# Performance work log

Hardware: AMD Instinct MI355X
Metric: run time of the kernel (lower is better)

## Reference

```python
import jax, jax.numpy as jnp
import numpy as np

M, D, NI, L, NPL, R, T = 2, 128, 131072, 4, 2048, 8, 32
N = NI + L * NPL  # total DAG nodes


def setup_inputs() -> dict:
    key = jax.random.key(0)
    ks = jax.random.split(key, 18)
    thax = jax.random.randint(ks[0], (NI,), 0, T)
    sine = jax.random.uniform(ks[1], (NI,), jnp.float32)
    # parents of layer-l deriv nodes index any node built earlier (topological)
    raw = jax.random.randint(ks[2], (L, NPL, 2), 0, 2**30)
    bounds = jnp.array([NI + l * NPL for l in range(L)])[:, None, None]
    par = raw % bounds
    ridx = jax.random.randint(ks[3], (L, NPL), 0, R)
    pos = jax.random.uniform(ks[4], (N,), jnp.float32) + 0.01
    neg = jax.random.uniform(ks[5], (N,), jnp.float32) + 0.01
    s = 0.05
    return {
        'thax': thax, 'sine': sine, 'par': par, 'ridx': ridx,
        'pos': pos, 'neg': neg,
        'init_table': jax.random.normal(ks[6], (M, T, D)) * s,
        's_vec': jax.random.normal(ks[7], (M, D)) * s,
        'W1': jax.random.normal(ks[8], (M, R, 2 * D, D)) * s,
        'b1': jax.random.normal(ks[9], (M, R, D)) * s,
        'W2': jax.random.normal(ks[10], (M, R, D, D)) * s,
        'b2': jax.random.normal(ks[11], (M, R, D)) * s,
        'tweaks': jax.random.normal(ks[12], (M, 1, 2)) * s,
        'We1': jax.random.normal(ks[13], (M, D, D)) * s,
        'be1': jax.random.normal(ks[14], (M, D)) * s,
        'we2': jax.random.normal(ks[15], (M, D)) * s,
        'be2': jax.random.normal(ks[16], (M,)) * s,
    }


def reference(thax, sine, par, ridx, pos, neg, init_table, s_vec,
              W1, b1, W2, b2, tweaks, We1, be1, we2, be2):
    # init nodes: thax embedding + sine embellishment (per model)
    emb0 = init_table[:, thax, :] + sine[None, :, None] * s_vec[:, None, :]  # [M,NI,D]
    store = jnp.zeros((M, N, D), emb0.dtype).at[:, :NI].set(emb0)
    # topological layers of deriv nodes: gather parents, rule-indexed 2-layer MLP
    for l in range(L):
        p, r = par[l], ridx[l]
        cat = store[:, p].reshape(M, NPL, 2 * D)               # gather parents
        h = jax.nn.relu(jnp.einsum('mnc,mncd->mnd', cat, W1[:, r]) + b1[:, r])
        out = (jnp.einsum('mnd,mnde->mne', h, W2[:, r]) + b2[:, r]
               + tweaks[:, 0, 1][:, None, None])
        store = store.at[:, NI + l * NPL: NI + (l + 1) * NPL].set(out)
    # eval_net: per-node scalar logit (+ per-problem tweak)
    he = jax.nn.relu(jnp.einsum('mnd,mde->mne', store, We1) + be1[:, None, :])
    logit = jnp.einsum('mnd,md->mn', he, we2) + be2[:, None] + tweaks[:, 0, 0][:, None]
    tot_pos, tot_neg = pos.sum(), neg.sum()
    pw = tot_neg / tot_pos  # POS_WEIGHT_EXTRA = 1.0
    gold = pos / (pos + neg)
    w = pos + neg
    # BCEWithLogitsLoss(pos_weight=pw) per node, weighted by (pos+neg)
    bce = -(pw * gold[None] * jax.nn.log_sigmoid(logit)
            + (1.0 - gold[None]) * jax.nn.log_sigmoid(-logit))
    loss = (w[None] * bce).sum(axis=1)                          # [M]
    posOK = jnp.where(logit >= 0, pos[None], 0.0).sum(axis=1)
    negOK = jnp.where(logit < 0, neg[None], 0.0).sum(axis=1)
    return (loss, posOK, negOK, tot_pos, tot_neg)
```

## Files before the change

### kernel.cpp

```cpp
#include <hip/hip_runtime.h>
#include <hip/hip_bf16.h>

#define M_ 2
#define D_ 128
#define NI_ 131072
#define L_ 4
#define NPL_ 2048
#define R_ 8
#define T_ 32
#define N_ (NI_ + L_ * NPL_)
#define ND_ (L_ * NPL_)
#define PSTRIDE_ 1792
#define PUSED_ 1665
#define FCAP_ 1280
#define SCAP_ 512
#define CCAP_ 24

typedef __bf16 bf16x8 __attribute__((ext_vector_type(8)));
typedef float f32x4 __attribute__((ext_vector_type(4)));
typedef unsigned short u16x4 __attribute__((ext_vector_type(4)));

#define OFF_W2T    0u
#define OFF_WE1T   524288u
#define OFF_TAB    589824u
#define OFF_SVEC   606208u
#define OFF_EA2    606720u
#define OFF_EWB    639488u
#define OFF_PA     641536u
#define OFF_PB     655872u
#define OFF_PPOK   670208u
#define OFF_PNOK   684544u
#define OFF_PTP    698880u
#define OFF_PTN    706048u
#define OFF_G      713216u
#define OFF_FLIST  1253888u
#define OFF_SLIST  1294848u
#define OFF_CFG    1296896u

__device__ __forceinline__ unsigned short f2bu(float f) {
  unsigned int u = __float_as_uint(f);
  u += 0x7fffu + ((u >> 16) & 1u);
  return (unsigned short)(u >> 16);
}
__device__ __forceinline__ float bfu2f(unsigned short u) {
  return __uint_as_float((unsigned int)u << 16);
}
__device__ __forceinline__ bf16x8 ldb8(const unsigned short* p) {
  return *reinterpret_cast<const bf16x8*>(p);
}

__global__ __launch_bounds__(256) void megaprep_kernel(
    const float* W1, const float* W2, const float* We1,
    const float* init_table, const float* s_vec,
    const float* b1, const float* be1, const float* we2,
    const int* ridx, const int* par,
    unsigned short* W2T, unsigned short* We1T,
    unsigned short* tab, unsigned short* svec,
    float* G, float* EA2, float* EWB,
    int* fastlist, int* slowlist, int* cfg, unsigned int* pzero) {
  __shared__ float smem[1056];
  __shared__ int lcnt;
  int job = blockIdx.x;
  int tid = threadIdx.x;

  if (job < 9) {
    int* out; int cap;
    if (job < 8) { out = fastlist + job * FCAP_; cap = FCAP_; }
    else         { out = slowlist;               cap = SCAP_; }
    if (tid == 0) lcnt = 0;
    __syncthreads();
    int lane = tid & 63;
    unsigned long long lmask_lt = (1ull << lane) - 1ull;
    for (int g = tid; g < ND_; g += 256) {
      int p0 = par[2 * g], p1 = par[2 * g + 1];
      bool fast = (p0 < NI_) && (p1 < NI_);
      bool match = (job < 8) ? (fast && ridx[g] == job) : (!fast);
      unsigned long long mask = __ballot(match);
      if (mask) {
        int leader = __ffsll((unsigned long long)mask) - 1;
        int pre = __popcll(mask & lmask_lt);
        int base_ = 0;
        if (lane == leader) base_ = atomicAdd(&lcnt, __popcll(mask));
        base_ = __shfl(base_, leader, 64);
        if (match) {
          int idx = base_ + pre;
          if (idx < cap) out[idx] = g;
        }
      }
    }
    __syncthreads();
    if (tid == 0) {
      int c = lcnt; if (c > cap) c = cap;
      cfg[job] = c;
    }
  } else if (job == 9) {
    for (int i = tid; i < 17920; i += 256) pzero[i] = 0u;
  } else if (job == 10) {
    for (int i = tid; i < 8448; i += 256) {
      if (i < 8192) tab[i] = f2bu(init_table[i]);
      else svec[i - 8192] = f2bu(s_vec[i - 8192]);
    }
  } else if (job < 45) {
    int q = job - 11;
    int m = q / 17, t = (q % 17) * 2 + (tid >> 7);
    int e = tid & 127;
    if (t <= 32) {
      const float* vec = (t < 32) ? &init_table[(size_t)(m * T_ + t) * D_]
                                  : &s_vec[(size_t)m * D_];
      const float* w = &We1[(size_t)m * D_ * D_];
      float acc = 0.f;
#pragma unroll 8
      for (int d = 0; d < 128; ++d) acc = fmaf(vec[d], w[d * D_ + e], acc);
      if (t < 32) {
        EA2[m * 4096 + ((e >> 1) * 32 + t) * 2 + (e & 1)] = acc + be1[m * D_ + e];
      } else {
        EWB[(m * D_ + e) * 2 + 0] = acc;
        EWB[(m * D_ + e) * 2 + 1] = we2[m * D_ + e];
      }
    }
  } else if (job < 573) {
    int q = job - 45;
    int t = q / 16, mr = q & 15;
    int m = mr >> 3;
    int slot = tid >> 7, e = tid & 127;
    const float* vec = (t < 32) ? &init_table[(size_t)(m * T_ + t) * D_]
                                : &s_vec[(size_t)m * D_];
    if (tid < 128) smem[tid] = vec[tid];
    __syncthreads();
    const float* w = &W1[((size_t)mr * 256 + slot * 128) * D_];
    float acc = 0.f;
#pragma unroll 8
    for (int c = 0; c < 128; ++c) acc = fmaf(smem[c], w[c * D_ + e], acc);
    if (slot == 0 && t < 32) acc += b1[mr * D_ + e];
    G[((size_t)(mr * 2 + slot) * 33 + t) * D_ + e] = acc;
  } else {
    int q0 = job - 573;
    const float* src; unsigned short* dst;
    int rblk, cblk;
    if (q0 < 256) {
      int z = q0 >> 4;
      src = W2 + (size_t)z * 16384; dst = W2T + (size_t)z * 16384;
      rblk = (q0 & 15) >> 2; cblk = q0 & 3;
    } else {
      int q = q0 - 256; int z = q >> 4;
      src = We1 + (size_t)z * 16384; dst = We1T + (size_t)z * 16384;
      rblk = (q & 15) >> 2; cblk = q & 3;
    }
    int r0 = rblk * 32, c0 = cblk * 32;
    float (*tile)[33] = (float(*)[33])smem;
    int tx = tid & 31, ty = tid >> 5;
#pragma unroll
    for (int k = 0; k < 4; ++k)
      tile[ty + 8 * k][tx] = src[(size_t)(r0 + ty + 8 * k) * D_ + c0 + tx];
    __syncthreads();
#pragma unroll
    for (int k = 0; k < 4; ++k)
      dst[(size_t)(c0 + ty + 8 * k) * D_ + r0 + tx] = f2bu(tile[tx][ty + 8 * k]);
  }
}

__global__ __launch_bounds__(256) void main_kernel(
    const int* thax, const float* sine, const int* par, const int* ridx,
    const float* pos, const float* neg,
    const float* W1, const float* b1, const float* b2, const float* tweaks,
    const float* G, const unsigned short* W2T, const unsigned short* We1T,
    const unsigned short* tab, const unsigned short* svec,
    const float* EA2, const float* EWB,
    const float* be1, const float* we2, const float* be2,
    const int* cfg, const int* fastlist, const int* slowlist,
    float* pA, float* pB, float* pPok, float* pNok, float* pTp, float* pTn) {
  __shared__ float sbuf[4448];
  int bid = blockIdx.x;
  int tid = threadIdx.x;
  int w = tid >> 6, lane = tid & 63;

  if (bid < 1280) {
    int m = bid / 640, q = bid % 640;
    int r = q / 80, tile = q % 80;
    int cnt = cfg[r];
    int base = tile * 16;
    if (base >= cnt) return;
    unsigned short* h_lds = (unsigned short*)sbuf;
    int*   t0a  = (int*)(sbuf + 1024);
    int*   t1a  = t0a + 16;
    float* s0a  = (float*)(t1a + 16);
    float* s1a  = s0a + 16;
    int*   gida = (int*)(s1a + 16);
    float* red2 = sbuf + 1104;
    if (tid < 16) {
      int loc = base + tid; if (loc >= cnt) loc = cnt - 1;
      int gid = fastlist[r * FCAP_ + loc];
      int p0 = par[2 * gid], p1 = par[2 * gid + 1];
      t0a[tid] = thax[p0]; s0a[tid] = sine[p0];
      t1a[tid] = thax[p1]; s1a[tid] = sine[p1];
      gida[tid] = gid;
    }
    __syncthreads();
    const float* Gm = &G[(size_t)(m * R_ + r) * 8448];
    {
      int row = tid >> 4, seg = tid & 15, d0 = seg * 8;
      int t0 = t0a[row], t1 = t1a[row];
      float s0 = s0a[row], s1 = s1a[row];
      const float* pa = &Gm[t0 * 128 + d0];
      const float* pb = &Gm[(33 + t1) * 128 + d0];
      const float* pu = &Gm[4096 + d0];
      const float* pv = &Gm[8320 + d0];
      bf16x8 hv;
#pragma unroll
      for (int half = 0; half < 2; ++half) {
        float4 a = *(const float4*)(pa + half * 4);
        float4 b = *(const float4*)(pb + half * 4);
        float4 u = *(const float4*)(pu + half * 4);
        float4 v = *(const float4*)(pv + half * 4);
        hv[half * 4 + 0] = (__bf16)fmaxf(a.x + b.x + s0 * u.x + s1 * v.x, 0.f);
        hv[half * 4 + 1] = (__bf16)fmaxf(a.y + b.y + s0 * u.y + s1 * v.y, 0.f);
        hv[half * 4 + 2] = (__bf16)fmaxf(a.z + b.z + s0 * u.z + s1 * v.z, 0.f);
        hv[half * 4 + 3] = (__bf16)fmaxf(a.w + b.w + s0 * u.w + s1 * v.w, 0.f);
      }
      *(bf16x8*)&h_lds[row * 128 + (d0 ^ ((row & 7) << 3))] = hv;
    }
    __syncthreads();
    int l15 = lane & 15, l4 = lane >> 4;
    const unsigned short* w2b = &W2T[(size_t)(m * R_ + r) * D_ * D_];
    f32x4 acc[2];
    acc[0] = (f32x4){0.f, 0.f, 0.f, 0.f};
    acc[1] = (f32x4){0.f, 0.f, 0.f, 0.f};
#pragma unroll
    for (int kc = 0; kc < 4; ++kc) {
      int d0 = kc * 32 + l4 * 8;
      bf16x8 a2 = ldb8(&h_lds[l15 * 128 + (d0 ^ ((l15 & 7) << 3))]);
#pragma unroll
      for (int f = 0; f < 2; ++f) {
        int fg = w * 2 + f;
        bf16x8 b = ldb8(&w2b[(fg * 16 + l15) * D_ + d0]);
        acc[f] = __builtin_amdgcn_mfma_f32_16x16x32_bf16(a2, b, acc[f], 0, 0, 0);
      }
    }
    float tw1 = tweaks[m * 2 + 1];
    const float* b2v = &b2[(m * R_ + r) * D_];
    __syncthreads();
#pragma unroll
    for (int i = 0; i < 4; ++i) {
      int row = l4 * 4 + i;
#pragma unroll
      for (int f = 0; f < 2; ++f) {
        int e = (w * 2 + f) * 16 + l15;
        h_lds[row * 128 + (e ^ ((row & 7) << 3))] = f2bu(acc[f][i] + b2v[e] + tw1);
      }
    }
    __syncthreads();
    f32x4 ae[2];
    ae[0] = (f32x4){0.f, 0.f, 0.f, 0.f};
    ae[1] = (f32x4){0.f, 0.f, 0.f, 0.f};
    const unsigned short* we1b = &We1T[(size_t)m * D_ * D_];
#pragma unroll
    for (int kc = 0; kc < 4; ++kc) {
      int d0 = kc * 32 + l4 * 8;
      bf16x8 a2 = ldb8(&h_lds[l15 * 128 + (d0 ^ ((l15 & 7) << 3))]);
#pragma unroll
      for (int f = 0; f < 2; ++f) {
        int fg = w * 2 + f;
        bf16x8 b = ldb8(&we1b[(fg * 16 + l15) * D_ + d0]);
        ae[f] = __builtin_amdgcn_mfma_f32_16x16x32_bf16(a2, b, ae[f], 0, 0, 0);
      }
    }
    float part[4] = {0.f, 0.f, 0.f, 0.f};
#pragma unroll
    for (int f = 0; f < 2; ++f) {
      int e = (w * 2 + f) * 16 + l15;
      float bb = be1[m * D_ + e];
      float wv = we2[m * D_ + e];
#pragma unroll
      for (int i = 0; i < 4; ++i) {
        float he = ae[f][i] + bb;
        he = he > 0.f ? he : 0.f;
        part[i] += he * wv;
      }
    }
#pragma unroll
    for (int mask = 1; mask < 16; mask <<= 1) {
#pragma unroll
      for (int i = 0; i < 4; ++i) part[i] += __shfl_xor(part[i], mask, 64);
    }
    if (l15 == 0) {
#pragma unroll
      for (int i = 0; i < 4; ++i) red2[w * 16 + l4 * 4 + i] = part[i];
    }
    __syncthreads();
    if (tid < 16) {
      int g = base + tid;
      float v6[4] = {0.f, 0.f, 0.f, 0.f};
      if (g < cnt) {
        float logit = red2[tid] + red2[16 + tid] + red2[32 + tid] + red2[48 + tid]
                    + be2[m] + tweaks[m * 2 + 0];
        int grow = NI_ + gida[tid];
        float p_ = pos[grow], n_ = neg[grow];
        float lse = log1pf(__expf(-fabsf(logit)));
        v6[0] = p_ * (fmaxf(-logit, 0.f) + lse);
        v6[1] = n_ * (fmaxf(logit, 0.f) + lse);
        v6[2] = logit >= 0.f ? p_ : 0.f;
        v6[3] = logit < 0.f ? n_ : 0.f;
      }
#pragma unroll
      for (int mask = 1; mask < 16; mask <<= 1) {
#pragma unroll
        for (int qq = 0; qq < 4; ++qq) v6[qq] += __shfl_xor(v6[qq], mask, 64);
      }
      if (tid == 0) {
        int slot = 512 + r * 80 + tile;
        pA[m * PSTRIDE_ + slot] = v6[0];
        pB[m * PSTRIDE_ + slot] = v6[1];
        pPok[m * PSTRIDE_ + slot] = v6[2];
        pNok[m * PSTRIDE_ + slot] = v6[3];
      }
    }
  } else if (bid < 2304) {
    int q = bid - 1280;
    int m = q >> 9, xb = q & 511;
    float* lea = sbuf;
    float* lwb = sbuf + 4096;
    float* red = sbuf + 4352;
    for (int i = tid; i < 4096; i += 256) lea[i] = EA2[m * 4096 + i];
    if (tid < 256) lwb[tid] = EWB[m * 256 + tid];
    __syncthreads();
    int row = xb * 256 + tid;
    int t = thax[row];
    float s = sine[row];
    float acc = 0.f;
#pragma unroll 8
    for (int p = 0; p < 64; ++p) {
      float2 ea = *(const float2*)&lea[(p * 32 + t) * 2];
      float4 wb = *(const float4*)&lwb[p * 4];
      float x0 = fmaf(s, wb.x, ea.x); x0 = fmaxf(x0, 0.f);
      acc = fmaf(x0, wb.y, acc);
      float x1 = fmaf(s, wb.z, ea.y); x1 = fmaxf(x1, 0.f);
      acc = fmaf(x1, wb.w, acc);
    }
    float logit = acc + be2[m] + tweaks[m * 2 + 0];
    float p_ = pos[row], n_ = neg[row];
    float lse = log1pf(__expf(-fabsf(logit)));
    float v[6];
    v[0] = p_ * (fmaxf(-logit, 0.f) + lse);
    v[1] = n_ * (fmaxf(logit, 0.f) + lse);
    v[2] = logit >= 0.f ? p_ : 0.f;
    v[3] = logit < 0.f ? n_ : 0.f;
    v[4] = p_; v[5] = n_;
#pragma unroll
    for (int mask = 1; mask < 64; mask <<= 1) {
#pragma unroll
      for (int k = 0; k < 6; ++k) v[k] += __shfl_xor(v[k], mask, 64);
    }
    if (lane == 0) {
#pragma unroll
      for (int k = 0; k < 6; ++k) red[k * 16 + w] = v[k];
    }
    __syncthreads();
    if (tid == 0) {
      float t6[6];
#pragma unroll
      for (int k = 0; k < 6; ++k)
        t6[k] = red[k * 16 + 0] + red[k * 16 + 1] + red[k * 16 + 2] + red[k * 16 + 3];
      pA[m * PSTRIDE_ + xb] = t6[0];
      pB[m * PSTRIDE_ + xb] = t6[1];
      pPok[m * PSTRIDE_ + xb] = t6[2];
      pNok[m * PSTRIDE_ + xb] = t6[3];
      if (m == 0) { pTp[xb] = t6[4]; pTn[xb] = t6[5]; }
    }
  } else if (bid < 2306) {
    int j = bid - 2304;
    float* red = sbuf;
    const float* src = j ? neg : pos;
    float s = 0.f;
    for (int i = NI_ + tid; i < N_; i += 256) s += src[i];
#pragma unroll
    for (int mask = 1; mask < 64; mask <<= 1) s += __shfl_xor(s, mask, 64);
    if (lane == 0) red[w] = s;
    __syncthreads();
    if (tid == 0) {
      float t = red[0] + red[1] + red[2] + red[3];
      if (j == 0) pTp[1152] = t; else pTn[1152] = t;
    }
  } else {
    int q = bid - 2306;
    int m = q >> 9, si = q & 511;
    if (si >= cfg[8]) return;
    int*   list  = (int*)sbuf;
    int*   meta  = (int*)(sbuf + 24);
    unsigned short* catl = (unsigned short*)(sbuf + 32);
    float* hbuf  = sbuf + 160;
    float* hp0   = sbuf + 288;
    float* hp1   = sbuf + 416;
    unsigned short* cache = (unsigned short*)(sbuf + 544);

    int g_row = slowlist[si];
    if (tid == 0) {
      int nn = 0;
      list[nn++] = g_row;
      for (int i = 0; i < nn; ++i) {
        int g = list[i];
        for (int s = 0; s < 2; ++s) {
          int p = par[2 * g + s];
          if (p >= NI_) {
            int pg = p - NI_;
            bool found = false;
            for (int jj = 0; jj < nn; ++jj) if (list[jj] == pg) { found = true; break; }
            if (!found && nn < CCAP_) list[nn++] = pg;
          }
        }
      }
      for (int i = 1; i < nn; ++i) {
        int v = list[i]; int jj = i - 1;
        while (jj >= 0 && list[jj] > v) { list[jj + 1] = list[jj]; --jj; }
        list[jj + 1] = v;
      }
      meta[0] = nn;
    }
    __syncthreads();
    int NN = meta[0];
    float tw1 = tweaks[m * 2 + 1];
    for (int j = 0; j < NN; ++j) {
      int g = list[j];
      int r = ridx[g];
      int p0 = par[2 * g], p1 = par[2 * g + 1];
      bool fastn = (p0 < NI_) && (p1 < NI_);
      if (fastn) {
        if (tid < 128) {
          int d = tid;
          const float* Gm = &G[(size_t)(m * R_ + r) * 8448];
          float hv = Gm[thax[p0] * 128 + d] + Gm[(33 + thax[p1]) * 128 + d]
                   + sine[p0] * Gm[4096 + d] + sine[p1] * Gm[8320 + d];
          hbuf[d] = bfu2f(f2bu(fmaxf(hv, 0.f)));
        }
        __syncthreads();
      } else {
        if (tid == 0) {
          int s0 = -1, s1 = -1;
          if (p0 >= NI_) for (int jj = 0; jj < j; ++jj) if (list[jj] == p0 - NI_) { s0 = jj; break; }
          if (p1 >= NI_) for (int jj = 0; jj < j; ++jj) if (list[jj] == p1 - NI_) { s1 = jj; break; }
          meta[1] = s0; meta[2] = s1;
        }
        __syncthreads();
        {
          int c = tid; int p = (c < 128) ? p0 : p1; int cc = c & 127;
          int slot = (c < 128) ? meta[1] : meta[2];
          unsigned short v;
          if (p < NI_) {
            float tv = bfu2f(tab[(m * T_ + thax[p]) * D_ + cc])
                     + sine[p] * bfu2f(svec[m * D_ + cc]);
            v = f2bu(tv);
          } else {
            v = cache[slot * 128 + cc];
          }
          catl[c] = v;
        }
        __syncthreads();
        int d = tid & 127, half = tid >> 7;
        const float* w1r = &W1[(((size_t)(m * R_ + r)) * 256 + half * 128) * D_];
        float acc = 0.f;
#pragma unroll 8
        for (int c = 0; c < 128; ++c)
          acc = fmaf(bfu2f(catl[half * 128 + c]), w1r[(size_t)c * D_ + d], acc);
        if (half == 0) hp0[d] = acc; else hp1[d] = acc;
        __syncthreads();
        if (tid < 128) {
          float hv = b1[(m * R_ + r) * D_ + tid] + hp0[tid] + hp1[tid];
          hbuf[tid] = bfu2f(f2bu(fmaxf(hv, 0.f)));
        }
        __syncthreads();
      }
      {
        int e = tid & 127, half = tid >> 7;
        const u16x4* w2r4 = (const u16x4*)&W2T[((size_t)(m * R_ + r) * D_ + e) * D_ + half * 64];
        float acc = 0.f;
#pragma unroll
        for (int dd = 0; dd < 16; ++dd) {
          u16x4 wv = w2r4[dd];
          int db = half * 64 + dd * 4;
          acc = fmaf(bfu2f(wv[0]), hbuf[db + 0], acc);
          acc = fmaf(bfu2f(wv[1]), hbuf[db + 1], acc);
          acc = fmaf(bfu2f(wv[2]), hbuf[db + 2], acc);
          acc = fmaf(bfu2f(wv[3]), hbuf[db + 3], acc);
        }
        if (half == 0) hp0[e] = acc; else hp1[e] = acc;
      }
      __syncthreads();
      if (tid < 128) {
        float o = hp0[tid] + hp1[tid] + b2[(m * R_ + r) * D_ + tid] + tw1;
        cache[j * 128 + tid] = f2bu(o);
      }
      __syncthreads();
    }
    int jr = NN - 1;
    {
      int e = tid & 127, half = tid >> 7;
      const u16x4* wer4 = (const u16x4*)&We1T[((size_t)m * D_ + e) * D_ + half * 64];
      float acc = 0.f;
#pragma unroll
      for (int dd = 0; dd < 16; ++dd) {
        u16x4 wv = wer4[dd];
        int db = half * 64 + dd * 4;
        acc = fmaf(bfu2f(wv[0]), bfu2f(cache[jr * 128 + db + 0]), acc);
        acc = fmaf(bfu2f(wv[1]), bfu2f(cache[jr * 128 + db + 1]), acc);
        acc = fmaf(bfu2f(wv[2]), bfu2f(cache[jr * 128 + db + 2]), acc);
        acc = fmaf(bfu2f(wv[3]), bfu2f(cache[jr * 128 + db + 3]), acc);
      }
      if (half == 0) hp0[e] = acc; else hp1[e] = acc;
    }
    __syncthreads();
    if (tid < 128) {
      float he = hp0[tid] + hp1[tid] + be1[m * D_ + tid];
      he = he > 0.f ? he : 0.f;
      hbuf[tid] = he * we2[m * D_ + tid];
    }
    __syncthreads();
    if (tid < 64) {
      float s = hbuf[tid] + hbuf[tid + 64];
#pragma unroll
      for (int mask = 1; mask < 64; mask <<= 1) s += __shfl_xor(s, mask, 64);
      if (tid == 0) {
        float logit = s + be2[m] + tweaks[m * 2 + 0];
        int grow = NI_ + g_row;
        float p_ = pos[grow], n_ = neg[grow];
        float lse = log1pf(__expf(-fabsf(logit)));
        int slot = 1153 + si;
        pA[m * PSTRIDE_ + slot] = p_ * (fmaxf(-logit, 0.f) + lse);
        pB[m * PSTRIDE_ + slot] = n_ * (fmaxf(logit, 0.f) + lse);
        pPok[m * PSTRIDE_ + slot] = logit >= 0.f ? p_ : 0.f;
        pNok[m * PSTRIDE_ + slot] = logit < 0.f ? n_ : 0.f;
      }
    }
  }
}

__global__ __launch_bounds__(256) void finalize_kernel(
    const float* pA, const float* pB, const float* pPok, const float* pNok,
    const float* pTp, const float* pTn, float* out) {
  __shared__ float lred[10][4];
  const float* srcs[10] = {pA, pA + PSTRIDE_, pB, pB + PSTRIDE_,
                           pPok, pPok + PSTRIDE_, pNok, pNok + PSTRIDE_,
                           pTp, pTn};
  int tid = threadIdx.x;
  int w = tid >> 6, lane = tid & 63;
#pragma unroll
  for (int q = 0; q < 10; ++q) {
    float s = 0.f;
    for (int i = tid; i < PUSED_; i += 256) s += srcs[q][i];
#pragma unroll
    for (int mask = 1; mask < 64; mask <<= 1) s += __shfl_xor(s, mask, 64);
    if (lane == 0) lred[q][w] = s;
  }
  __syncthreads();
  if (tid == 0) {
    float totals[10];
#pragma unroll
    for (int q = 0; q < 10; ++q)
      totals[q] = lred[q][0] + lred[q][1] + lred[q][2] + lred[q][3];
    float tp = totals[8], tn = totals[9];
    float pw = tn / tp;
    out[0] = pw * totals[0] + totals[2];
    out[1] = pw * totals[1] + totals[3];
    out[2] = totals[4]; out[3] = totals[5];
    out[4] = totals[6]; out[5] = totals[7];
    out[6] = tp; out[7] = tn;
  }
}

extern "C" void kernel_launch(void* const* d_in, const int* in_sizes, int n_in,
                              void* d_out, int out_size, void* d_ws, size_t ws_size,
                              hipStream_t stream) {
  const int*   thax = (const int*)d_in[0];
  const float* sine = (const float*)d_in[1];
  const int*   par  = (const int*)d_in[2];
  const int*   ridx = (const int*)d_in[3];
  const float* pos  = (const float*)d_in[4];
  const float* neg  = (const float*)d_in[5];
  const float* init_table = (const float*)d_in[6];
  const float* s_vec = (const float*)d_in[7];
  const float* W1 = (const float*)d_in[8];
  const float* b1 = (const float*)d_in[9];
  const float* W2 = (const float*)d_in[10];
  const float* b2 = (const float*)d_in[11];
  const float* tweaks = (const float*)d_in[12];
  const float* We1 = (const float*)d_in[13];
  const float* be1 = (const float*)d_in[14];
  const float* we2 = (const float*)d_in[15];
  const float* be2 = (const float*)d_in[16];

  char* ws = (char*)d_ws;
  unsigned short* W2T  = (unsigned short*)(ws + OFF_W2T);
  unsigned short* We1T = (unsigned short*)(ws + OFF_WE1T);
  unsigned short* tab  = (unsigned short*)(ws + OFF_TAB);
  unsigned short* svec = (unsigned short*)(ws + OFF_SVEC);
  float* EA2  = (float*)(ws + OFF_EA2);
  float* EWB  = (float*)(ws + OFF_EWB);
  float* pA   = (float*)(ws + OFF_PA);
  float* pB   = (float*)(ws + OFF_PB);
  float* pPok = (float*)(ws + OFF_PPOK);
  float* pNok = (float*)(ws + OFF_PNOK);
  float* pTp  = (float*)(ws + OFF_PTP);
  float* pTn  = (float*)(ws + OFF_PTN);
  float* G    = (float*)(ws + OFF_G);
  int* fastlist = (int*)(ws + OFF_FLIST);
  int* slowlist = (int*)(ws + OFF_SLIST);
  int* cfg      = (int*)(ws + OFF_CFG);

  megaprep_kernel<<<861, 256, 0, stream>>>(
      W1, W2, We1, init_table, s_vec, b1, be1, we2, ridx, par,
      W2T, We1T, tab, svec, G, EA2, EWB,
      fastlist, slowlist, cfg, (unsigned int*)pA);
  main_kernel<<<3330, 256, 0, stream>>>(
      thax, sine, par, ridx, pos, neg, W1, b1, b2, tweaks,
      G, W2T, We1T, tab, svec, EA2, EWB, be1, we2, be2,
      cfg, fastlist, slowlist,
      pA, pB, pPok, pNok, pTp, pTn);
  finalize_kernel<<<1, 256, 0, stream>>>(pA, pB, pPok, pNok, pTp, pTn,
                                         (float*)d_out);
}
```

Before: 92.43 us.

## Process slow-path dependency chains one per wavefront instead of one per block

The slow path, which recomputes each deep-layer node's ancestor chain, now gives each 64-lane wavefront its own chain and LDS slice. Block-wide __syncthreads are replaced by per-wave lgkmcnt waits, and the grid for that section shrinks fourfold. This is meant to cut barrier overhead and idle threads on the latency-bound serial chains. In exchange each lane does longer serial dot products (256- and 128-length loops), and the chain cap drops from 24 to 16, which could truncate deep chains.

Result: slower. 112.1 us (+21.3%).

```diff
diff --git a/kernel.cpp b/kernel.cpp
--- a/kernel.cpp
+++ b/kernel.cpp
@@ -14,11 +14,11 @@
 #define PUSED_ 1665
 #define FCAP_ 1280
 #define SCAP_ 512
-#define CCAP_ 24
+#define CCAP_ 16
+#define WSL_ 1312
 
 typedef __bf16 bf16x8 __attribute__((ext_vector_type(8)));
 typedef float f32x4 __attribute__((ext_vector_type(4)));
-typedef unsigned short u16x4 __attribute__((ext_vector_type(4)));
 
 #define OFF_W2T    0u
 #define OFF_WE1T   524288u
@@ -48,6 +48,10 @@
 __device__ __forceinline__ bf16x8 ldb8(const unsigned short* p) {
   return *reinterpret_cast<const bf16x8*>(p);
 }
+#define WAVE_FENCE() do { \
+  asm volatile("s_waitcnt lgkmcnt(0)" ::: "memory"); \
+  __builtin_amdgcn_sched_barrier(0); \
+} while (0)
 
 __global__ __launch_bounds__(256) void megaprep_kernel(
     const float* W1, const float* W2, const float* We1,
@@ -169,7 +173,7 @@
     const float* be1, const float* we2, const float* be2,
     const int* cfg, const int* fastlist, const int* slowlist,
     float* pA, float* pB, float* pPok, float* pNok, float* pTp, float* pTn) {
-  __shared__ float sbuf[4448];
+  __shared__ float sbuf[4 * WSL_];
   int bid = blockIdx.x;
   int tid = threadIdx.x;
   int w = tid >> 6, lane = tid & 63;
@@ -381,153 +385,122 @@
       if (j == 0) pTp[1152] = t; else pTn[1152] = t;
     }
   } else {
-    int q = bid - 2306;
-    int m = q >> 9, si = q & 511;
+    int widx = (bid - 2306) * 4 + w;
+    int m = widx >> 9, si = widx & 511;
     if (si >= cfg[8]) return;
-    int*   list  = (int*)sbuf;
-    int*   meta  = (int*)(sbuf + 24);
-    unsigned short* catl = (unsigned short*)(sbuf + 32);
-    float* hbuf  = sbuf + 160;
-    float* hp0   = sbuf + 288;
-    float* hp1   = sbuf + 416;
-    unsigned short* cache = (unsigned short*)(sbuf + 544);
+    int*   ilist = (int*)&sbuf[w * WSL_];
+    unsigned short* cat = (unsigned short*)&sbuf[w * WSL_ + 18];
+    float* hbuf = &sbuf[w * WSL_ + 146];
+    unsigned short* cache = (unsigned short*)&sbuf[w * WSL_ + 274];
 
     int g_row = slowlist[si];
-    if (tid == 0) {
+    if (lane == 0) {
       int nn = 0;
-      list[nn++] = g_row;
+      ilist[nn++] = g_row;
       for (int i = 0; i < nn; ++i) {
-        int g = list[i];
+        int g = ilist[i];
         for (int s = 0; s < 2; ++s) {
           int p = par[2 * g + s];
           if (p >= NI_) {
             int pg = p - NI_;
             bool found = false;
-            for (int jj = 0; jj < nn; ++jj) if (list[jj] == pg) { found = true; break; }
-            if (!found && nn < CCAP_) list[nn++] = pg;
+            for (int jj = 0; jj < nn; ++jj) if (ilist[jj] == pg) { found = true; break; }
+            if (!found && nn < CCAP_) ilist[nn++] = pg;
           }
         }
       }
       for (int i = 1; i < nn; ++i) {
-        int v = list[i]; int jj = i - 1;
-        while (jj >= 0 && list[jj] > v) { list[jj + 1] = list[jj]; --jj; }
-        list[jj + 1] = v;
-      }
-      meta[0] = nn;
-    }
-    __syncthreads();
-    int NN = meta[0];
+        int v = ilist[i]; int jj = i - 1;
+        while (jj >= 0 && ilist[jj] > v) { ilist[jj + 1] = ilist[jj]; --jj; }
+        ilist[jj + 1] = v;
+      }
+      ilist[16] = nn;
+    }
+    WAVE_FENCE();
+    int NN = ilist[16];
     float tw1 = tweaks[m * 2 + 1];
     for (int j = 0; j < NN; ++j) {
-      int g = list[j];
+      int g = ilist[j];
       int r = ridx[g];
       int p0 = par[2 * g], p1 = par[2 * g + 1];
       bool fastn = (p0 < NI_) && (p1 < NI_);
       if (fastn) {
-        if (tid < 128) {
-          int d = tid;
-          const float* Gm = &G[(size_t)(m * R_ + r) * 8448];
-          float hv = Gm[thax[p0] * 128 + d] + Gm[(33 + thax[p1]) * 128 + d]
-                   + sine[p0] * Gm[4096 + d] + sine[p1] * Gm[8320 + d];
+        const float* Gm = &G[(size_t)(m * R_ + r) * 8448];
+        int t0 = thax[p0], t1 = thax[p1];
+        float s0 = sine[p0], s1 = sine[p1];
+#pragma unroll
+        for (int k = 0; k < 2; ++k) {
+          int d = lane + k * 64;
+          float hv = Gm[t0 * 128 + d] + Gm[(33 + t1) * 128 + d]
+                   + s0 * Gm[4096 + d] + s1 * Gm[8320 + d];
           hbuf[d] = bfu2f(f2bu(fmaxf(hv, 0.f)));
         }
-        __syncthreads();
       } else {
-        if (tid == 0) {
-          int s0 = -1, s1 = -1;
-          if (p0 >= NI_) for (int jj = 0; jj < j; ++jj) if (list[jj] == p0 - NI_) { s0 = jj; break; }
-          if (p1 >= NI_) for (int jj = 0; jj < j; ++jj) if (list[jj] == p1 - NI_) { s1 = jj; break; }
-          meta[1] = s0; meta[2] = s1;
-        }
-        __syncthreads();
-        {
-          int c = tid; int p = (c < 128) ? p0 : p1; int cc = c & 127;
-          int slot = (c < 128) ? meta[1] : meta[2];
+        int s0s = -1, s1s = -1;
+        if (p0 >= NI_) for (int jj = 0; jj < j; ++jj) if (ilist[jj] == p0 - NI_) { s0s = jj; break; }
+        if (p1 >= NI_) for (int jj = 0; jj < j; ++jj) if (ilist[jj] == p1 - NI_) { s1s = jj; break; }
+#pragma unroll
+        for (int k = 0; k < 4; ++k) {
+          int c = lane * 4 + k;
+          int p = (c < 128) ? p0 : p1; int cc = c & 127;
+          int slot = (c < 128) ? s0s : s1s;
           unsigned short v;
           if (p < NI_) {
-            float tv = bfu2f(tab[(m * T_ + thax[p]) * D_ + cc])
-                     + sine[p] * bfu2f(svec[m * D_ + cc]);
-            v = f2bu(tv);
+            v = f2bu(bfu2f(tab[(m * T_ + thax[p]) * D_ + cc])
+                     + sine[p] * bfu2f(svec[m * D_ + cc]));
           } else {
             v = cache[slot * 128 + cc];
           }
-          catl[c] = v;
+          cat[c] = v;
         }
-        __syncthreads();
-        int d = tid & 127, half = tid >> 7;
-        const float* w1r = &W1[(((size_t)(m * R_ + r)) * 256 + half * 128) * D_];
+        WAVE_FENCE();
+        const float* w1r = &W1[((size_t)(m * R_ + r)) * 256 * D_];
+#pragma unroll
+        for (int k = 0; k < 2; ++k) {
+          int d = lane + k * 64;
+          float acc = b1[(m * R_ + r) * D_ + d];
+          for (int c = 0; c < 256; ++c)
+            acc = fmaf(bfu2f(cat[c]), w1r[(size_t)c * D_ + d], acc);
+          hbuf[d] = bfu2f(f2bu(fmaxf(acc, 0.f)));
+        }
+      }
+      WAVE_FENCE();
+#pragma unroll
+      for (int k = 0; k < 2; ++k) {
+        int e = lane + k * 64;
+        const unsigned short* w2r = &W2T[((size_t)(m * R_ + r) * D_ + e) * D_];
         float acc = 0.f;
-#pragma unroll 8
-        for (int c = 0; c < 128; ++c)
-          acc = fmaf(bfu2f(catl[half * 128 + c]), w1r[(size_t)c * D_ + d], acc);
-        if (half == 0) hp0[d] = acc; else hp1[d] = acc;
-        __syncthreads();
-        if (tid < 128) {
-          float hv = b1[(m * R_ + r) * D_ + tid] + hp0[tid] + hp1[tid];
-          hbuf[tid] = bfu2f(f2bu(fmaxf(hv, 0.f)));
-        }
-        __syncthreads();
-      }
-      {
-        int e = tid & 127, half = tid >> 7;
-        const u16x4* w2r4 = (const u16x4*)&W2T[((size_t)(m * R_ + r) * D_ + e) * D_ + half * 64];
-        float acc = 0.f;
-#pragma unroll
-        for (int dd = 0; dd < 16; ++dd) {
-          u16x4 wv = w2r4[dd];
-          int db = half * 64 + dd * 4;
-          acc = fmaf(bfu2f(wv[0]), hbuf[db + 0], acc);
-          acc = fmaf(bfu2f(wv[1]), hbuf[db + 1], acc);
-          acc = fmaf(bfu2f(wv[2]), hbuf[db + 2], acc);
-          acc = fmaf(bfu2f(wv[3]), hbuf[db + 3], acc);
-        }
-        if (half == 0) hp0[e] = acc; else hp1[e] = acc;
-      }
-      __syncthreads();
-      if (tid < 128) {
-        float o = hp0[tid] + hp1[tid] + b2[(m * R_ + r) * D_ + tid] + tw1;
-        cache[j * 128 + tid] = f2bu(o);
-      }
-      __syncthreads();
+        for (int d = 0; d < 128; ++d)
+          acc = fmaf(bfu2f(w2r[d]), hbuf[d], acc);
+        cache[j * 128 + e] = f2bu(acc + b2[(m * R_ + r) * D_ + e] + tw1);
+      }
+      WAVE_FENCE();
     }
     int jr = NN - 1;
-    {
-      int e = tid & 127, half = tid >> 7;
-      const u16x4* wer4 = (const u16x4*)&We1T[((size_t)m * D_ + e) * D_ + half * 64];
+    float part = 0.f;
+#pragma unroll
+    for (int k = 0; k < 2; ++k) {
+      int e = lane + k * 64;
+      const unsigned short* wer = &We1T[((size_t)m * D_ + e) * D_];
       float acc = 0.f;
-#pragma unroll
-      for (int dd = 0; dd < 16; ++dd) {
-        u16x4 wv = wer4[dd];
-        int db = half * 64 + dd * 4;
-        acc = fmaf(bfu2f(wv[0]), bfu2f(cache[jr * 128 + db + 0]), acc);
-        acc = fmaf(bfu2f(wv[1]), bfu2f(cache[jr * 128 + db + 1]), acc);
-        acc = fmaf(bfu2f(wv[2]), bfu2f(cache[jr * 128 + db + 2]), acc);
-        acc = fmaf(bfu2f(wv[3]), bfu2f(cache[jr * 128 + db + 3]), acc);
-      }
-      if (half == 0) hp0[e] = acc; else hp1[e] = acc;
-    }
-    __syncthreads();
-    if (tid < 128) {
-      float he = hp0[tid] + hp1[tid] + be1[m * D_ + tid];
+      for (int d = 0; d < 128; ++d)
+        acc = fmaf(bfu2f(wer[d]), bfu2f(cache[jr * 128 + d]), acc);
+      float he = acc + be1[m * D_ + e];
       he = he > 0.f ? he : 0.f;
-      hbuf[tid] = he * we2[m * D_ + tid];
-    }
-    __syncthreads();
-    if (tid < 64) {
-      float s = hbuf[tid] + hbuf[tid + 64];
-#pragma unroll
-      for (int mask = 1; mask < 64; mask <<= 1) s += __shfl_xor(s, mask, 64);
-      if (tid == 0) {
-        float logit = s + be2[m] + tweaks[m * 2 + 0];
-        int grow = NI_ + g_row;
-        float p_ = pos[grow], n_ = neg[grow];
-        float lse = log1pf(__expf(-fabsf(logit)));
-        int slot = 1153 + si;
-        pA[m * PSTRIDE_ + slot] = p_ * (fmaxf(-logit, 0.f) + lse);
-        pB[m * PSTRIDE_ + slot] = n_ * (fmaxf(logit, 0.f) + lse);
-        pPok[m * PSTRIDE_ + slot] = logit >= 0.f ? p_ : 0.f;
-        pNok[m * PSTRIDE_ + slot] = logit < 0.f ? n_ : 0.f;
-      }
+      part += he * we2[m * D_ + e];
+    }
+#pragma unroll
+    for (int mask = 1; mask < 64; mask <<= 1) part += __shfl_xor(part, mask, 64);
+    if (lane == 0) {
+      float logit = part + be2[m] + tweaks[m * 2 + 0];
+      int grow = NI_ + g_row;
+      float p_ = pos[grow], n_ = neg[grow];
+      float lse = log1pf(__expf(-fabsf(logit)));
+      int slot = 1153 + si;
+      pA[m * PSTRIDE_ + slot] = p_ * (fmaxf(-logit, 0.f) + lse);
+      pB[m * PSTRIDE_ + slot] = n_ * (fmaxf(logit, 0.f) + lse);
+      pPok[m * PSTRIDE_ + slot] = logit >= 0.f ? p_ : 0.f;
+      pNok[m * PSTRIDE_ + slot] = logit < 0.f ? n_ : 0.f;
     }
   }
 }
@@ -608,7 +581,7 @@
       W1, W2, We1, init_table, s_vec, b1, be1, we2, ridx, par,
       W2T, We1T, tab, svec, G, EA2, EWB,
       fastlist, slowlist, cfg, (unsigned int*)pA);
-  main_kernel<<<3330, 256, 0, stream>>>(
+  main_kernel<<<2562, 256, 0, stream>>>(
       thax, sine, par, ridx, pos, neg, W1, b1, b2, tweaks,
       G, W2T, We1T, tab, svec, EA2, EWB, be1, we2, be2,
       cfg, fastlist, slowlist,
```

## Batch G/EA2 precompute per weight slice and schedule slow-path blocks first

Applied to the files above, without the earlier changes.

The prep kernel's G and EA2 precompute is restructured. Each block now stages all 33 embedding vectors in shared memory and reuses each loaded W1/We1 element across 17 token rows, instead of running one block per token row. This cuts the prep grid from 861 to 333 blocks and removes redundant weight reads. The main kernel also reorders its block ranges so the long serial slow-path blocks launch first and overlap with the fast tiles, at the cost of higher register pressure and larger shared memory in prep.

Result: faster. 88.57 us, median of 2 (-4.2%).

```diff
diff --git a/kernel.cpp b/kernel.cpp
--- a/kernel.cpp
+++ b/kernel.cpp
@@ -58,7 +58,7 @@
     unsigned short* tab, unsigned short* svec,
     float* G, float* EA2, float* EWB,
     int* fastlist, int* slowlist, int* cfg, unsigned int* pzero) {
-  __shared__ float smem[1056];
+  __shared__ float smem[4352];
   __shared__ int lcnt;
   int job = blockIdx.x;
   int tid = threadIdx.x;
@@ -93,48 +93,78 @@
       int c = lcnt; if (c > cap) c = cap;
       cfg[job] = c;
     }
-  } else if (job == 9) {
+  } else if (job < 41) {
+    int q = job - 9;
+    int mr = q >> 1, slot = q & 1;
+    int m = mr >> 3;
+    for (int i = tid; i < 4352; i += 256) {
+      int t = i >> 7, c = i & 127;
+      smem[i] = (t < 32) ? init_table[(size_t)(m * T_ + t) * D_ + c]
+              : (t == 32) ? s_vec[(size_t)m * D_ + c] : 0.f;
+    }
+    __syncthreads();
+    int e = tid & 127, tg = tid >> 7;
+    int t0 = tg ? 17 : 0;
+    int nt = tg ? 16 : 17;
+    float acc[17];
+#pragma unroll
+    for (int k = 0; k < 17; ++k) acc[k] = 0.f;
+    const float* w1base = &W1[(size_t)(mr * 256 + slot * 128) * D_ + e];
+#pragma unroll 4
+    for (int c = 0; c < 128; ++c) {
+      float w1c = w1base[(size_t)c * D_];
+#pragma unroll
+      for (int k = 0; k < 17; ++k)
+        acc[k] = fmaf(smem[(t0 + k) * 128 + c], w1c, acc[k]);
+    }
+    float bb = b1[mr * D_ + e];
+    for (int k = 0; k < nt; ++k) {
+      int t = t0 + k;
+      float v = acc[k];
+      if (slot == 0 && t < 32) v += bb;
+      G[((size_t)(mr * 2 + slot) * 33 + t) * D_ + e] = v;
+    }
+  } else if (job < 43) {
+    int m = job - 41;
+    for (int i = tid; i < 4352; i += 256) {
+      int t = i >> 7, c = i & 127;
+      smem[i] = (t < 32) ? init_table[(size_t)(m * T_ + t) * D_ + c]
+              : (t == 32) ? s_vec[(size_t)m * D_ + c] : 0.f;
+    }
+    __syncthreads();
+    int e = tid & 127, tg = tid >> 7;
+    int t0 = tg ? 17 : 0;
+    int nt = tg ? 16 : 17;
+    float acc[17];
+#pragma unroll
+    for (int k = 0; k < 17; ++k) acc[k] = 0.f;
+    const float* webase = &We1[(size_t)m * D_ * D_ + e];
+#pragma unroll 4
+    for (int c = 0; c < 128; ++c) {
+      float wc = webase[(size_t)c * D_];
+#pragma unroll
+      for (int k = 0; k < 17; ++k)
+        acc[k] = fmaf(smem[(t0 + k) * 128 + c], wc, acc[k]);
+    }
+    float bev = be1[m * D_ + e];
+    for (int k = 0; k < nt; ++k) {
+      int t = t0 + k;
+      if (t < 32) {
+        EA2[m * 4096 + ((e >> 1) * 32 + t) * 2 + (e & 1)] = acc[k] + bev;
+      } else {
+        EWB[(m * D_ + e) * 2 + 0] = acc[k];
+        EWB[(m * D_ + e) * 2 + 1] = we2[m * D_ + e];
+      }
+    }
+  } else if (job == 43) {
     for (int i = tid; i < 17920; i += 256) pzero[i] = 0u;
-  } else if (job == 10) {
+  } else if (job == 44) {
     for (int i = tid; i < 8448; i += 256) {
       if (i < 8192) tab[i] = f2bu(init_table[i]);
       else svec[i - 8192] = f2bu(s_vec[i - 8192]);
     }
-  } else if (job < 45) {
-    int q = job - 11;
-    int m = q / 17, t = (q % 17) * 2 + (tid >> 7);
-    int e = tid & 127;
-    if (t <= 32) {
-      const float* vec = (t < 32) ? &init_table[(size_t)(m * T_ + t) * D_]
-                                  : &s_vec[(size_t)m * D_];
-      const float* w = &We1[(size_t)m * D_ * D_];
-      float acc = 0.f;
-#pragma unroll 8
-      for (int d = 0; d < 128; ++d) acc = fmaf(vec[d], w[d * D_ + e], acc);
-      if (t < 32) {
-        EA2[m * 4096 + ((e >> 1) * 32 + t) * 2 + (e & 1)] = acc + be1[m * D_ + e];
-      } else {
-        EWB[(m * D_ + e) * 2 + 0] = acc;
-        EWB[(m * D_ + e) * 2 + 1] = we2[m * D_ + e];
-      }
-    }
-  } else if (job < 573) {
-    int q = job - 45;
-    int t = q / 16, mr = q & 15;
-    int m = mr >> 3;
-    int slot = tid >> 7, e = tid & 127;
-    const float* vec = (t < 32) ? &init_table[(size_t)(m * T_ + t) * D_]
-                                : &s_vec[(size_t)m * D_];
-    if (tid < 128) smem[tid] = vec[tid];
-    __syncthreads();
-    const float* w = &W1[((size_t)mr * 256 + slot * 128) * D_];
-    float acc = 0.f;
-#pragma unroll 8
-    for (int c = 0; c < 128; ++c) acc = fmaf(smem[c], w[c * D_ + e], acc);
-    if (slot == 0 && t < 32) acc += b1[mr * D_ + e];
-    G[((size_t)(mr * 2 + slot) * 33 + t) * D_ + e] = acc;
   } else {
-    int q0 = job - 573;
+    int q0 = job - 45;
     const float* src; unsigned short* dst;
     int rblk, cblk;
     if (q0 < 256) {
@@ -174,215 +204,8 @@
   int tid = threadIdx.x;
   int w = tid >> 6, lane = tid & 63;
 
-  if (bid < 1280) {
-    int m = bid / 640, q = bid % 640;
-    int r = q / 80, tile = q % 80;
-    int cnt = cfg[r];
-    int base = tile * 16;
-    if (base >= cnt) return;
-    unsigned short* h_lds = (unsigned short*)sbuf;
-    int*   t0a  = (int*)(sbuf + 1024);
-    int*   t1a  = t0a + 16;
-    float* s0a  = (float*)(t1a + 16);
-    float* s1a  = s0a + 16;
-    int*   gida = (int*)(s1a + 16);
-    float* red2 = sbuf + 1104;
-    if (tid < 16) {
-      int loc = base + tid; if (loc >= cnt) loc = cnt - 1;
-      int gid = fastlist[r * FCAP_ + loc];
-      int p0 = par[2 * gid], p1 = par[2 * gid + 1];
-      t0a[tid] = thax[p0]; s0a[tid] = sine[p0];
-      t1a[tid] = thax[p1]; s1a[tid] = sine[p1];
-      gida[tid] = gid;
-    }
-    __syncthreads();
-    const float* Gm = &G[(size_t)(m * R_ + r) * 8448];
-    {
-      int row = tid >> 4, seg = tid & 15, d0 = seg * 8;
-      int t0 = t0a[row], t1 = t1a[row];
-      float s0 = s0a[row], s1 = s1a[row];
-      const float* pa = &Gm[t0 * 128 + d0];
-      const float* pb = &Gm[(33 + t1) * 128 + d0];
-      const float* pu = &Gm[4096 + d0];
-      const float* pv = &Gm[8320 + d0];
-      bf16x8 hv;
-#pragma unroll
-      for (int half = 0; half < 2; ++half) {
-        float4 a = *(const float4*)(pa + half * 4);
-        float4 b = *(const float4*)(pb + half * 4);
-        float4 u = *(const float4*)(pu + half * 4);
-        float4 v = *(const float4*)(pv + half * 4);
-        hv[half * 4 + 0] = (__bf16)fmaxf(a.x + b.x + s0 * u.x + s1 * v.x, 0.f);
-        hv[half * 4 + 1] = (__bf16)fmaxf(a.y + b.y + s0 * u.y + s1 * v.y, 0.f);
-        hv[half * 4 + 2] = (__bf16)fmaxf(a.z + b.z + s0 * u.z + s1 * v.z, 0.f);
-        hv[half * 4 + 3] = (__bf16)fmaxf(a.w + b.w + s0 * u.w + s1 * v.w, 0.f);
-      }
-      *(bf16x8*)&h_lds[row * 128 + (d0 ^ ((row & 7) << 3))] = hv;
-    }
-    __syncthreads();
-    int l15 = lane & 15, l4 = lane >> 4;
-    const unsigned short* w2b = &W2T[(size_t)(m * R_ + r) * D_ * D_];
-    f32x4 acc[2];
-    acc[0] = (f32x4){0.f, 0.f, 0.f, 0.f};
-    acc[1] = (f32x4){0.f, 0.f, 0.f, 0.f};
-#pragma unroll
-    for (int kc = 0; kc < 4; ++kc) {
-      int d0 = kc * 32 + l4 * 8;
-      bf16x8 a2 = ldb8(&h_lds[l15 * 128 + (d0 ^ ((l15 & 7) << 3))]);
-#pragma unroll
-      for (int f = 0; f < 2; ++f) {
-        int fg = w * 2 + f;
-        bf16x8 b = ldb8(&w2b[(fg * 16 + l15) * D_ + d0]);
-        acc[f] = __builtin_amdgcn_mfma_f32_16x16x32_bf16(a2, b, acc[f], 0, 0, 0);
-      }
-    }
-    float tw1 = tweaks[m * 2 + 1];
-    const float* b2v = &b2[(m * R_ + r) * D_];
-    __syncthreads();
-#pragma unroll
-    for (int i = 0; i < 4; ++i) {
-      int row = l4 * 4 + i;
-#pragma unroll
-      for (int f = 0; f < 2; ++f) {
-        int e = (w * 2 + f) * 16 + l15;
-        h_lds[row * 128 + (e ^ ((row & 7) << 3))] = f2bu(acc[f][i] + b2v[e] + tw1);
-      }
-    }
-    __syncthreads();
-    f32x4 ae[2];
-    ae[0] = (f32x4){0.f, 0.f, 0.f, 0.f};
-    ae[1] = (f32x4){0.f, 0.f, 0.f, 0.f};
-    const unsigned short* we1b = &We1T[(size_t)m * D_ * D_];
-#pragma unroll
-    for (int kc = 0; kc < 4; ++kc) {
-      int d0 = kc * 32 + l4 * 8;
-      bf16x8 a2 = ldb8(&h_lds[l15 * 128 + (d0 ^ ((l15 & 7) << 3))]);
-#pragma unroll
-      for (int f = 0; f < 2; ++f) {
-        int fg = w * 2 + f;
-        bf16x8 b = ldb8(&we1b[(fg * 16 + l15) * D_ + d0]);
-        ae[f] = __builtin_amdgcn_mfma_f32_16x16x32_bf16(a2, b, ae[f], 0, 0, 0);
-      }
-    }
-    float part[4] = {0.f, 0.f, 0.f, 0.f};
-#pragma unroll
-    for (int f = 0; f < 2; ++f) {
-      int e = (w * 2 + f) * 16 + l15;
-      float bb = be1[m * D_ + e];
-      float wv = we2[m * D_ + e];
-#pragma unroll
-      for (int i = 0; i < 4; ++i) {
-        float he = ae[f][i] + bb;
-        he = he > 0.f ? he : 0.f;
-        part[i] += he * wv;
-      }
-    }
-#pragma unroll
-    for (int mask = 1; mask < 16; mask <<= 1) {
-#pragma unroll
-      for (int i = 0; i < 4; ++i) part[i] += __shfl_xor(part[i], mask, 64);
-    }
-    if (l15 == 0) {
-#pragma unroll
-      for (int i = 0; i < 4; ++i) red2[w * 16 + l4 * 4 + i] = part[i];
-    }
-    __syncthreads();
-    if (tid < 16) {
-      int g = base + tid;
-      float v6[4] = {0.f, 0.f, 0.f, 0.f};
-      if (g < cnt) {
-        float logit = red2[tid] + red2[16 + tid] + red2[32 + tid] + red2[48 + tid]
-                    + be2[m] + tweaks[m * 2 + 0];
-        int grow = NI_ + gida[tid];
-        float p_ = pos[grow], n_ = neg[grow];
-        float lse = log1pf(__expf(-fabsf(logit)));
-        v6[0] = p_ * (fmaxf(-logit, 0.f) + lse);
-        v6[1] = n_ * (fmaxf(logit, 0.f) + lse);
-        v6[2] = logit >= 0.f ? p_ : 0.f;
-        v6[3] = logit < 0.f ? n_ : 0.f;
-      }
-#pragma unroll
-      for (int mask = 1; mask < 16; mask <<= 1) {
-#pragma unroll
-        for (int qq = 0; qq < 4; ++qq) v6[qq] += __shfl_xor(v6[qq], mask, 64);
-      }
-      if (tid == 0) {
-        int slot = 512 + r * 80 + tile;
-        pA[m * PSTRIDE_ + slot] = v6[0];
-        pB[m * PSTRIDE_ + slot] = v6[1];
-        pPok[m * PSTRIDE_ + slot] = v6[2];
-        pNok[m * PSTRIDE_ + slot] = v6[3];
-      }
-    }
-  } else if (bid < 2304) {
-    int q = bid - 1280;
-    int m = q >> 9, xb = q & 511;
-    float* lea = sbuf;
-    float* lwb = sbuf + 4096;
-    float* red = sbuf + 4352;
-    for (int i = tid; i < 4096; i += 256) lea[i] = EA2[m * 4096 + i];
-    if (tid < 256) lwb[tid] = EWB[m * 256 + tid];
-    __syncthreads();
-    int row = xb * 256 + tid;
-    int t = thax[row];
-    float s = sine[row];
-    float acc = 0.f;
-#pragma unroll 8
-    for (int p = 0; p < 64; ++p) {
-      float2 ea = *(const float2*)&lea[(p * 32 + t) * 2];
-      float4 wb = *(const float4*)&lwb[p * 4];
-      float x0 = fmaf(s, wb.x, ea.x); x0 = fmaxf(x0, 0.f);
-      acc = fmaf(x0, wb.y, acc);
-      float x1 = fmaf(s, wb.z, ea.y); x1 = fmaxf(x1, 0.f);
-      acc = fmaf(x1, wb.w, acc);
-    }
-    float logit = acc + be2[m] + tweaks[m * 2 + 0];
-    float p_ = pos[row], n_ = neg[row];
-    float lse = log1pf(__expf(-fabsf(logit)));
-    float v[6];
-    v[0] = p_ * (fmaxf(-logit, 0.f) + lse);
-    v[1] = n_ * (fmaxf(logit, 0.f) + lse);
-    v[2] = logit >= 0.f ? p_ : 0.f;
-    v[3] = logit < 0.f ? n_ : 0.f;
-    v[4] = p_; v[5] = n_;
-#pragma unroll
-    for (int mask = 1; mask < 64; mask <<= 1) {
-#pragma unroll
-      for (int k = 0; k < 6; ++k) v[k] += __shfl_xor(v[k], mask, 64);
-    }
-    if (lane == 0) {
-#pragma unroll
-      for (int k = 0; k < 6; ++k) red[k * 16 + w] = v[k];
-    }
-    __syncthreads();
-    if (tid == 0) {
-      float t6[6];
-#pragma unroll
-      for (int k = 0; k < 6; ++k)
-        t6[k] = red[k * 16 + 0] + red[k * 16 + 1] + red[k * 16 + 2] + red[k * 16 + 3];
-      pA[m * PSTRIDE_ + xb] = t6[0];
-      pB[m * PSTRIDE_ + xb] = t6[1];
-      pPok[m * PSTRIDE_ + xb] = t6[2];
-      pNok[m * PSTRIDE_ + xb] = t6[3];
-      if (m == 0) { pTp[xb] = t6[4]; pTn[xb] = t6[5]; }
-    }
-  } else if (bid < 2306) {
-    int j = bid - 2304;
-    float* red = sbuf;
-    const float* src = j ? neg : pos;
-    float s = 0.f;
-    for (int i = NI_ + tid; i < N_; i += 256) s += src[i];
-#pragma unroll
-    for (int mask = 1; mask < 64; mask <<= 1) s += __shfl_xor(s, mask, 64);
-    if (lane == 0) red[w] = s;
-    __syncthreads();
-    if (tid == 0) {
-      float t = red[0] + red[1] + red[2] + red[3];
-      if (j == 0) pTp[1152] = t; else pTn[1152] = t;
-    }
-  } else {
-    int q = bid - 2306;
-    int m = q >> 9, si = q & 511;
+  if (bid < 1024) {
+    int m = bid >> 9, si = bid & 511;
     if (si >= cfg[8]) return;
     int*   list  = (int*)sbuf;
     int*   meta  = (int*)(sbuf + 24);
@@ -529,6 +352,213 @@
         pNok[m * PSTRIDE_ + slot] = logit < 0.f ? n_ : 0.f;
       }
     }
+  } else if (bid < 2304) {
+    int fb = bid - 1024;
+    int m = fb / 640, q = fb % 640;
+    int r = q / 80, tile = q % 80;
+    int cnt = cfg[r];
+    int base = tile * 16;
+    if (base >= cnt) return;
+    unsigned short* h_lds = (unsigned short*)sbuf;
+    int*   t0a  = (int*)(sbuf + 1024);
+    int*   t1a  = t0a + 16;
+    float* s0a  = (float*)(t1a + 16);
+    float* s1a  = s0a + 16;
+    int*   gida = (int*)(s1a + 16);
+    float* red2 = sbuf + 1104;
+    if (tid < 16) {
+      int loc = base + tid; if (loc >= cnt) loc = cnt - 1;
+      int gid = fastlist[r * FCAP_ + loc];
+      int p0 = par[2 * gid], p1 = par[2 * gid + 1];
+      t0a[tid] = thax[p0]; s0a[tid] = sine[p0];
+      t1a[tid] = thax[p1]; s1a[tid] = sine[p1];
+      gida[tid] = gid;
+    }
+    __syncthreads();
+    const float* Gm = &G[(size_t)(m * R_ + r) * 8448];
+    {
+      int row = tid >> 4, seg = tid & 15, d0 = seg * 8;
+      int t0 = t0a[row], t1 = t1a[row];
+      float s0 = s0a[row], s1 = s1a[row];
+      const float* pa = &Gm[t0 * 128 + d0];
+      const float* pb = &Gm[(33 + t1) * 128 + d0];
+      const float* pu = &Gm[4096 + d0];
+      const float* pv = &Gm[8320 + d0];
+      bf16x8 hv;
+#pragma unroll
+      for (int half = 0; half < 2; ++half) {
+        float4 a = *(const float4*)(pa + half * 4);
+        float4 b = *(const float4*)(pb + half * 4);
+        float4 u = *(const float4*)(pu + half * 4);
+        float4 v = *(const float4*)(pv + half * 4);
+        hv[half * 4 + 0] = (__bf16)fmaxf(a.x + b.x + s0 * u.x + s1 * v.x, 0.f);
+        hv[half * 4 + 1] = (__bf16)fmaxf(a.y + b.y + s0 * u.y + s1 * v.y, 0.f);
+        hv[half * 4 + 2] = (__bf16)fmaxf(a.z + b.z + s0 * u.z + s1 * v.z, 0.f);
+        hv[half * 4 + 3] = (__bf16)fmaxf(a.w + b.w + s0 * u.w + s1 * v.w, 0.f);
+      }
+      *(bf16x8*)&h_lds[row * 128 + (d0 ^ ((row & 7) << 3))] = hv;
+    }
+    __syncthreads();
+    int l15 = lane & 15, l4 = lane >> 4;
+    const unsigned short* w2b = &W2T[(size_t)(m * R_ + r) * D_ * D_];
+    f32x4 acc[2];
+    acc[0] = (f32x4){0.f, 0.f, 0.f, 0.f};
+    acc[1] = (f32x4){0.f, 0.f, 0.f, 0.f};
+#pragma unroll
+    for (int kc = 0; kc < 4; ++kc) {
+      int d0 = kc * 32 + l4 * 8;
+      bf16x8 a2 = ldb8(&h_lds[l15 * 128 + (d0 ^ ((l15 & 7) << 3))]);
+#pragma unroll
+      for (int f = 0; f < 2; ++f) {
+        int fg = w * 2 + f;
+        bf16x8 b = ldb8(&w2b[(fg * 16 + l15) * D_ + d0]);
+        acc[f] = __builtin_amdgcn_mfma_f32_16x16x32_bf16(a2, b, acc[f], 0, 0, 0);
+      }
+    }
+    float tw1 = tweaks[m * 2 + 1];
+    const float* b2v = &b2[(m * R_ + r) * D_];
+    __syncthreads();
+#pragma unroll
+    for (int i = 0; i < 4; ++i) {
+      int row = l4 * 4 + i;
+#pragma unroll
+      for (int f = 0; f < 2; ++f) {
+        int e = (w * 2 + f) * 16 + l15;
+        h_lds[row * 128 + (e ^ ((row & 7) << 3))] = f2bu(acc[f][i] + b2v[e] + tw1);
+      }
+    }
+    __syncthreads();
+    f32x4 ae[2];
+    ae[0] = (f32x4){0.f, 0.f, 0.f, 0.f};
+    ae[1] = (f32x4){0.f, 0.f, 0.f, 0.f};
+    const unsigned short* we1b = &We1T[(size_t)m * D_ * D_];
+#pragma unroll
+    for (int kc = 0; kc < 4; ++kc) {
+      int d0 = kc * 32 + l4 * 8;
+      bf16x8 a2 = ldb8(&h_lds[l15 * 128 + (d0 ^ ((l15 & 7) << 3))]);
+#pragma unroll
+      for (int f = 0; f < 2; ++f) {
+        int fg = w * 2 + f;
+        bf16x8 b = ldb8(&we1b[(fg * 16 + l15) * D_ + d0]);
+        ae[f] = __builtin_amdgcn_mfma_f32_16x16x32_bf16(a2, b, ae[f], 0, 0, 0);
+      }
+    }
+    float part[4] = {0.f, 0.f, 0.f, 0.f};
+#pragma unroll
+    for (int f = 0; f < 2; ++f) {
+      int e = (w * 2 + f) * 16 + l15;
+      float bb = be1[m * D_ + e];
+      float wv = we2[m * D_ + e];
+#pragma unroll
+      for (int i = 0; i < 4; ++i) {
+        float he = ae[f][i] + bb;
+        he = he > 0.f ? he : 0.f;
+        part[i] += he * wv;
+      }
+    }
+#pragma unroll
+    for (int mask = 1; mask < 16; mask <<= 1) {
+#pragma unroll
+      for (int i = 0; i < 4; ++i) part[i] += __shfl_xor(part[i], mask, 64);
+    }
+    if (l15 == 0) {
+#pragma unroll
+      for (int i = 0; i < 4; ++i) red2[w * 16 + l4 * 4 + i] = part[i];
+    }
+    __syncthreads();
+    if (tid < 16) {
+      int g = base + tid;
+      float v6[4] = {0.f, 0.f, 0.f, 0.f};
+      if (g < cnt) {
+        float logit = red2[tid] + red2[16 + tid] + red2[32 + tid] + red2[48 + tid]
+                    + be2[m] + tweaks[m * 2 + 0];
+        int grow = NI_ + gida[tid];
+        float p_ = pos[grow], n_ = neg[grow];
+        float lse = log1pf(__expf(-fabsf(logit)));
+        v6[0] = p_ * (fmaxf(-logit, 0.f) + lse);
+        v6[1] = n_ * (fmaxf(logit, 0.f) + lse);
+        v6[2] = logit >= 0.f ? p_ : 0.f;
+        v6[3] = logit < 0.f ? n_ : 0.f;
+      }
+#pragma unroll
+      for (int mask = 1; mask < 16; mask <<= 1) {
+#pragma unroll
+        for (int qq = 0; qq < 4; ++qq) v6[qq] += __shfl_xor(v6[qq], mask, 64);
+      }
+      if (tid == 0) {
+        int slot = 512 + r * 80 + tile;
+        pA[m * PSTRIDE_ + slot] = v6[0];
+        pB[m * PSTRIDE_ + slot] = v6[1];
+        pPok[m * PSTRIDE_ + slot] = v6[2];
+        pNok[m * PSTRIDE_ + slot] = v6[3];
+      }
+    }
+  } else if (bid < 3328) {
+    int q = bid - 2304;
+    int m = q >> 9, xb = q & 511;
+    float* lea = sbuf;
+    float* lwb = sbuf + 4096;
+    float* red = sbuf + 4352;
+    for (int i = tid; i < 4096; i += 256) lea[i] = EA2[m * 4096 + i];
+    if (tid < 256) lwb[tid] = EWB[m * 256 + tid];
+    __syncthreads();
+    int row = xb * 256 + tid;
+    int t = thax[row];
+    float s = sine[row];
+    float acc = 0.f;
+#pragma unroll 8
+    for (int p = 0; p < 64; ++p) {
+      float2 ea = *(const float2*)&lea[(p * 32 + t) * 2];
+      float4 wb = *(const float4*)&lwb[p * 4];
+      float x0 = fmaf(s, wb.x, ea.x); x0 = fmaxf(x0, 0.f);
+      acc = fmaf(x0, wb.y, acc);
+      float x1 = fmaf(s, wb.z, ea.y); x1 = fmaxf(x1, 0.f);
+      acc = fmaf(x1, wb.w, acc);
+    }
+    float logit = acc + be2[m] + tweaks[m * 2 + 0];
+    float p_ = pos[row], n_ = neg[row];
+    float lse = log1pf(__expf(-fabsf(logit)));
+    float v[6];
+    v[0] = p_ * (fmaxf(-logit, 0.f) + lse);
+    v[1] = n_ * (fmaxf(logit, 0.f) + lse);
+    v[2] = logit >= 0.f ? p_ : 0.f;
+    v[3] = logit < 0.f ? n_ : 0.f;
+    v[4] = p_; v[5] = n_;
+#pragma unroll
+    for (int mask = 1; mask < 64; mask <<= 1) {
+#pragma unroll
+      for (int k = 0; k < 6; ++k) v[k] += __shfl_xor(v[k], mask, 64);
+    }
+    if (lane == 0) {
+#pragma unroll
+      for (int k = 0; k < 6; ++k) red[k * 16 + w] = v[k];
+    }
+    __syncthreads();
+    if (tid == 0) {
+      float t6[6];
+#pragma unroll
+      for (int k = 0; k < 6; ++k)
+        t6[k] = red[k * 16 + 0] + red[k * 16 + 1] + red[k * 16 + 2] + red[k * 16 + 3];
+      pA[m * PSTRIDE_ + xb] = t6[0];
+      pB[m * PSTRIDE_ + xb] = t6[1];
+      pPok[m * PSTRIDE_ + xb] = t6[2];
+      pNok[m * PSTRIDE_ + xb] = t6[3];
+      if (m == 0) { pTp[xb] = t6[4]; pTn[xb] = t6[5]; }
+    }
+  } else {
+    int j = bid - 3328;
+    float* red = sbuf;
+    const float* src = j ? neg : pos;
+    float s = 0.f;
+    for (int i = NI_ + tid; i < N_; i += 256) s += src[i];
+#pragma unroll
+    for (int mask = 1; mask < 64; mask <<= 1) s += __shfl_xor(s, mask, 64);
+    if (lane == 0) red[w] = s;
+    __syncthreads();
+    if (tid == 0) {
+      float t = red[0] + red[1] + red[2] + red[3];
+      if (j == 0) pTp[1152] = t; else pTn[1152] = t;
+    }
   }
 }
 
@@ -604,7 +634,7 @@
   int* slowlist = (int*)(ws + OFF_SLIST);
   int* cfg      = (int*)(ws + OFF_CFG);
 
-  megaprep_kernel<<<861, 256, 0, stream>>>(
+  megaprep_kernel<<<333, 256, 0, stream>>>(
       W1, W2, We1, init_table, s_vec, b1, be1, we2, ridx, par,
       W2T, We1T, tab, svec, G, EA2, EWB,
       fastlist, slowlist, cfg, (unsigned int*)pA);
```
